# Kernel tuning notes

Hardware: AMD Instinct MI355X
Metric: run time of the kernel (lower is better)

Reference implementation:

```python
import jax, jax.numpy as jnp
import numpy as np

N, E, G, P = 65536, 1048576, 512, 128   # nodes, edges, graphs, nodes per graph
K = 64                                   # sort-pool k (fixed in module)
NUM_CLASSES = 10
FEAT = 128


def _gcn_conv(x, W, b, src, dst):
    # PyG GCNConv: linear, add self-loops, symmetric-normalized aggregation, bias
    h = x @ W
    deg = jnp.ones((N,), x.dtype).at[dst].add(1.0)       # self-loop + in-degree
    dinv = jax.lax.rsqrt(deg)
    coef = (dinv[src] * dinv[dst])[:, None]
    agg = jax.ops.segment_sum(h[src] * coef, dst, num_segments=N)
    agg = agg + h * (dinv * dinv)[:, None]               # self-loop messages
    return agg + b


def setup_inputs() -> dict:
    key = jax.random.key(0)
    ks = jax.random.split(key, 12)
    x = jax.random.normal(ks[0], (N, FEAT), jnp.float32)
    src = jax.random.randint(ks[1], (E,), 0, N, dtype=jnp.int32)
    off = jax.random.randint(ks[2], (E,), 0, P, dtype=jnp.int32)
    dst = (src // P) * P + off                           # keep edges intra-graph
    edge_index = jnp.stack([src, dst])
    # balanced batch vector (implicit): node n belongs to graph n // P
    def lin(k, i, o):
        return jax.random.normal(k, (i, o), jnp.float32) / np.float32(np.sqrt(i))
    return {
        "x": x,
        "W1": lin(ks[3], FEAT, 128), "b1": jnp.zeros((128,), jnp.float32),
        "W2": lin(ks[4], 128, 64),   "b2": jnp.zeros((64,), jnp.float32),
        "W3": lin(ks[5], 64, 32),    "b3": jnp.zeros((32,), jnp.float32),
        "W4": lin(ks[6], 32, 32),    "b4": jnp.zeros((32,), jnp.float32),
        "W5": lin(ks[7], 256, 16).T, "b5": jnp.zeros((16,), jnp.float32),   # Conv1d(1,16,256,256)
        "W6": jax.random.normal(ks[8], (32, 16, 5), jnp.float32) * 0.1,      # Conv1d(16,32,5) OIH
        "b6": jnp.zeros((32,), jnp.float32),
        "Wf1": lin(ks[9], 896, 128), "bf1": jnp.zeros((128,), jnp.float32),
        "Wf2": lin(ks[10], 128, NUM_CLASSES), "bf2": jnp.zeros((NUM_CLASSES,), jnp.float32),
        "edge_index": edge_index,
    }


def reference(x, W1, b1, W2, b2, W3, b3, W4, b4, W5, b5, W6, b6,
              Wf1, bf1, Wf2, bf2, edge_index):
    src, dst = edge_index[0], edge_index[1]
    x1 = jnp.tanh(_gcn_conv(x, W1, b1, src, dst))
    x2 = jnp.tanh(_gcn_conv(x1, W2, b2, src, dst))
    x3 = jnp.tanh(_gcn_conv(x2, W3, b3, src, dst))
    x4 = jnp.tanh(_gcn_conv(x3, W4, b4, src, dst))
    h = jnp.concatenate([x1, x2, x3, x4], axis=-1)       # [N, 256]
    C = h.shape[-1]
    # global_sort_pool: balanced graphs of P nodes -> sort desc by last channel, take top-K
    hg = h.reshape(G, P, C)
    order = jnp.argsort(-hg[:, :, -1], axis=1)[:, :K]    # [G, K]
    pooled = jnp.take_along_axis(hg, order[:, :, None], axis=1)   # [G, K, C]
    # Conv1d(1, 16, 256, stride=256): kernel == stride == C, so per-node matmul
    z = jnp.einsum('gtj,cj->gct', pooled, W5) + b5[None, :, None]  # [G,16,64]
    z = jax.nn.relu(z)
    z = z.reshape(G, 16, -1, 2).max(axis=-1)                       # MaxPool1d(2,2) -> [G,16,32]
    z = jax.lax.conv_general_dilated(z, W6, (1,), 'VALID',
                                     dimension_numbers=('NCH', 'OIH', 'NCH'))
    z = jax.nn.relu(z + b6[None, :, None])                          # [G,32,28]
    z = z.reshape(G, -1)                                            # [G,896]
    out = jax.nn.relu(z @ Wf1 + bf1)
    # dropout is identity at eval time
    return jax.nn.log_softmax(out @ Wf2 + bf2, axis=-1)
```

## Files before the change

### kernel.cpp

```cpp
#include <hip/hip_runtime.h>

#define N_EDGES 1048576
#define N_GRAPH 512
#define REG     2560
#define MAXE    2560
#define PAD     64
#define CHUNK   2048
#define SBLK    (N_EDGES / CHUNK)

typedef __attribute__((ext_vector_type(4))) float floatx4;
typedef __attribute__((ext_vector_type(2))) float floatx2;
typedef __attribute__((ext_vector_type(4))) int intx4;

__global__ void zero_kernel(unsigned* __restrict__ p, int n) {
    int i = blockIdx.x * blockDim.x + threadIdx.x;
    if (i < n) p[i] = 0u;
}

__global__ void scatter_kernel(const int* __restrict__ src, const int* __restrict__ dst,
                               unsigned* __restrict__ cnt, unsigned short* __restrict__ ebuf) {
    __shared__ unsigned short sbuf[CHUNK];
    __shared__ unsigned short sg[CHUNK];
    __shared__ unsigned lhist[512];
    __shared__ unsigned lscan[512];
    __shared__ unsigned gbase[512];
    const int t = threadIdx.x;
    lhist[t] = 0; lhist[t + 256] = 0;
    __syncthreads();
    const intx4* s4 = (const intx4*)(src + blockIdx.x * CHUNK) + t * 2;
    const intx4* d4 = (const intx4*)(dst + blockIdx.x * CHUNK) + t * 2;
    unsigned short gg[8], pk[8], rr[8];
#pragma unroll
    for (int h = 0; h < 2; ++h) {
        intx4 sv = s4[h], dv = d4[h];
        int ss[4] = {sv.x, sv.y, sv.z, sv.w};
        int dd[4] = {dv.x, dv.y, dv.z, dv.w};
#pragma unroll
        for (int j = 0; j < 4; ++j) {
            unsigned g = ((unsigned)dd[j]) >> 7;
            gg[h * 4 + j] = (unsigned short)g;
            pk[h * 4 + j] = (unsigned short)((ss[j] & 127) | ((dd[j] & 127) << 8));
            rr[h * 4 + j] = (unsigned short)atomicAdd(&lhist[g], 1u);
        }
    }
    __syncthreads();
    unsigned a0 = lhist[t], a1 = lhist[t + 256];
    lscan[t] = a0; lscan[t + 256] = a1;
    __syncthreads();
    for (int d = 1; d < 512; d <<= 1) {
        unsigned v0 = (t >= d) ? lscan[t - d] : 0u;
        unsigned v1 = (t + 256 >= d) ? lscan[t + 256 - d] : 0u;
        __syncthreads();
        lscan[t] += v0; lscan[t + 256] += v1;
        __syncthreads();
    }
    lscan[t] -= a0; lscan[t + 256] -= a1;
    gbase[t]       = a0 ? atomicAdd(&cnt[(size_t)t * PAD], a0)         : 0u;
    gbase[t + 256] = a1 ? atomicAdd(&cnt[(size_t)(t + 256) * PAD], a1) : 0u;
    __syncthreads();
#pragma unroll
    for (int j = 0; j < 8; ++j) {
        unsigned pos = lscan[gg[j]] + rr[j];
        sbuf[pos] = pk[j]; sg[pos] = gg[j];
    }
    __syncthreads();
    for (int i = t; i < CHUNK; i += 256) {
        unsigned g = sg[i];
        unsigned pos = gbase[g] + (i - lscan[g]);
        if (pos < REG) ebuf[(size_t)g * REG + pos] = sbuf[i];
    }
}

template<int CIN, int COUT>
__device__ void gcn_matmul(const float* Xin, float* Xio,
                           const float* __restrict__ W, int tid)
{
    constexpr int CL  = COUT / 4;
    constexpr int NPT = 128 / (1024 / CL);
    const int grp = tid / CL, cl = tid % CL;

    float acc[NPT][4];
#pragma unroll
    for (int ni = 0; ni < NPT; ++ni)
#pragma unroll
        for (int j = 0; j < 4; ++j) acc[ni][j] = 0.f;

    for (int k = 0; k < CIN; k += 4) {
        floatx4 xv[NPT];
#pragma unroll
        for (int ni = 0; ni < NPT; ++ni)
            xv[ni] = *(const floatx4*)(Xin + (grp * NPT + ni) * CIN + k);
#pragma unroll
        for (int i = 0; i < 4; ++i) {
            floatx4 wv = *(const floatx4*)(W + (k + i) * COUT + cl * 4);
#pragma unroll
            for (int ni = 0; ni < NPT; ++ni)
#pragma unroll
                for (int j = 0; j < 4; ++j)
                    acc[ni][j] += xv[ni][i] * wv[j];
        }
    }
    __syncthreads();
#pragma unroll
    for (int ni = 0; ni < NPT; ++ni) {
        floatx4 v; v[0] = acc[ni][0]; v[1] = acc[ni][1]; v[2] = acc[ni][2]; v[3] = acc[ni][3];
        *(floatx4*)(Xio + (grp * NPT + ni) * COUT + cl * 4) = v;
    }
    __syncthreads();
}

template<int COUT, int CPT>
__device__ void gcn_agg(float* Xio, const float* __restrict__ Bv,
                        const float* __restrict__ dinv, const int* __restrict__ offs,
                        const float* __restrict__ epack, int tid)
{
    constexpr int TPN = COUT / CPT;
    constexpr int TOT = 128 * TPN;
    constexpr int NV  = CPT / 4;
    float v[NV][4];
    if (tid < TOT) {
        const int n = tid / TPN, cb = (tid % TPN) * CPT;
        float a[NV][4];
#pragma unroll
        for (int q = 0; q < NV; ++q)
#pragma unroll
            for (int j = 0; j < 4; ++j) a[q][j] = 0.f;
        const int o0 = offs[n], o1 = offs[n + 1];
        for (int p = o0; p < o1; ++p) {
            floatx2 e = *(const floatx2*)(epack + 2 * p);
            float cf = e[0];
            int s = (int)__float_as_uint(e[1]);
            const float* hr = Xio + s * COUT + cb;
#pragma unroll
            for (int q = 0; q < NV; ++q) {
                floatx4 h = *(const floatx4*)(hr + q * 4);
#pragma unroll
                for (int j = 0; j < 4; ++j) a[q][j] += h[j] * cf;
            }
        }
        float dn = dinv[n], dnn = dn * dn;
#pragma unroll
        for (int q = 0; q < NV; ++q) {
            floatx4 hs = *(const floatx4*)(Xio + n * COUT + cb + q * 4);
            floatx4 bv = *(const floatx4*)(Bv + cb + q * 4);
#pragma unroll
            for (int j = 0; j < 4; ++j) {
                float t2 = a[q][j] + hs[j] * dnn + bv[j];
                t2 = tanhf(t2);
                v[q][j] = fminf(fmaxf(t2, -1.0f), 1.0f);
            }
        }
    }
    __syncthreads();
    if (tid < TOT) {
        const int n = tid / TPN, cb = (tid % TPN) * CPT;
#pragma unroll
        for (int q = 0; q < NV; ++q) {
            floatx4 o; o[0] = v[q][0]; o[1] = v[q][1]; o[2] = v[q][2]; o[3] = v[q][3];
            *(floatx4*)(Xio + n * COUT + cb + q * 4) = o;
        }
    }
    __syncthreads();
}

__global__ __launch_bounds__(1024, 1) void mega_kernel(
    const float* __restrict__ x,
    const float* __restrict__ W1, const float* __restrict__ b1,
    const float* __restrict__ W2, const float* __restrict__ b2,
    const float* __restrict__ W3, const float* __restrict__ b3,
    const float* __restrict__ W4, const float* __restrict__ b4,
    const float* __restrict__ W5, const float* __restrict__ b5,
    const float* __restrict__ W6, const float* __restrict__ b6,
    const float* __restrict__ Wf1, const float* __restrict__ bf1,
    const float* __restrict__ Wf2, const float* __restrict__ bf2,
    const unsigned* __restrict__ cnt, const unsigned short* __restrict__ ebuf,
    float* __restrict__ out)
{
    __shared__ __align__(16) char pool[162048];
    int*   ldeg = (int*)(pool + 0);
    int*   offs = (int*)(pool + 512);
    float* dinv = (float*)(pool + 1040);
    float* key  = (float*)(pool + 1552);
    unsigned short* ord = (unsigned short*)(pool + 2064);
    float* epack = (float*)(pool + 2304);
    float* W5s   = (float*)(pool + 2304);
    float* X1   = (float*)(pool + 22784);
    float* X2   = (float*)(pool + 88320);
    float* X3   = (float*)(pool + 121088);
    float* X4   = (float*)(pool + 137472);
    float* SCR  = (float*)(pool + 153856);
    float* Zs   = SCR;
    float* ZMP  = SCR + 1024;
    float* Z896 = SCR;
    float* PART = SCR + 1024;
    float* FC1  = SCR + 896;
    float* LG   = SCR;

    const int g   = blockIdx.x;
    const int tid = threadIdx.x;
    int cnt_g = (int)cnt[(size_t)g * PAD];
    if (cnt_g > MAXE) cnt_g = MAXE;
    const unsigned short* eg = ebuf + (size_t)g * REG;

    unsigned short ev[3]; int ne = 0;
    for (int e = tid; e < cnt_g; e += 1024) ev[ne++] = eg[e];

    if (tid < 128) ldeg[tid] = 0;
    __syncthreads();
    for (int i = 0; i < ne; ++i) atomicAdd(&ldeg[(ev[i] >> 8) & 127], 1);
    __syncthreads();
    if (tid < 128) offs[tid + 1] = ldeg[tid];
    if (tid == 0)  offs[0] = 0;
    __syncthreads();
    for (int d = 1; d < 128; d <<= 1) {
        int v = 0;
        if (tid < 128 && tid >= d) v = offs[tid + 1 - d];
        __syncthreads();
        if (tid < 128 && tid >= d) offs[tid + 1] += v;
        __syncthreads();
    }
    if (tid < 128) {
        dinv[tid] = 1.0f / sqrtf((float)(1 + ldeg[tid]));
        ldeg[tid] = offs[tid];
    }
    __syncthreads();
    for (int i = 0; i < ne; ++i) {
        int dn_ = (ev[i] >> 8) & 127, sn = ev[i] & 127;
        int p = atomicAdd(&ldeg[dn_], 1);
        floatx2 e; e[0] = dinv[sn] * dinv[dn_]; e[1] = __uint_as_float((unsigned)sn);
        *(floatx2*)(epack + 2 * p) = e;
    }
    const float* xg = x + (size_t)g * 16384;
    for (int idx = tid; idx < 4096; idx += 1024)
        *(floatx4*)(X1 + idx * 4) = *(const floatx4*)(xg + idx * 4);
    __syncthreads();

    gcn_matmul<128, 128>(X1, X1, W1, tid);
    gcn_agg<128, 16>(X1, b1, dinv, offs, epack, tid);
    gcn_matmul<128,  64>(X1, X2, W2, tid);
    gcn_agg< 64,  8>(X2, b2, dinv, offs, epack, tid);
    gcn_matmul< 64,  32>(X2, X3, W3, tid);
    gcn_agg< 32,  8>(X3, b3, dinv, offs, epack, tid);
    gcn_matmul< 32,  32>(X3, X4, W4, tid);
    gcn_agg< 32,  8>(X4, b4, dinv, offs, epack, tid);

    if (tid < 128) key[tid] = X4[tid * 32 + 31];
    if (tid < 64)  ord[tid] = (unsigned short)tid;
    __syncthreads();
    for (int idx = tid; idx < 4096; idx += 1024) W5s[idx] = W5[idx];
    __syncthreads();
    if (tid < 128) {
        float myk = key[tid];
        int r = 0;
        for (int j = 0; j < 128; ++j) {
            float kj = key[j];
            r += (kj > myk) || (kj == myk && j < tid);
        }
        if (r < 64) ord[r] = (unsigned short)tid;
    }
    __syncthreads();

    {
        int q = tid >> 6, t = tid & 63;
        int node = ord[t] & 127;
        float z0 = b5[q];
        const float* w5a = W5s + q * 256;
        floatx4 zv = {0.f, 0.f, 0.f, 0.f};
        for (int jj = 0; jj < 32; ++jj) {
            int j = (jj + t) & 31;
            floatx4 pv = *(const floatx4*)(X1 + node * 128 + j * 4);
            floatx4 wv = *(const floatx4*)(w5a + j * 4);
#pragma unroll
            for (int u = 0; u < 4; ++u) zv[u] += pv[u] * wv[u];
        }
        for (int jj = 0; jj < 16; ++jj) {
            int j = (jj + t) & 15;
            floatx4 pv = *(const floatx4*)(X2 + node * 64 + j * 4);
            floatx4 wv = *(const floatx4*)(w5a + 128 + j * 4);
#pragma unroll
            for (int u = 0; u < 4; ++u) zv[u] += pv[u] * wv[u];
        }
        for (int jj = 0; jj < 8; ++jj) {
            int j = (jj + t) & 7;
            floatx4 pv = *(const floatx4*)(X3 + node * 32 + j * 4);
            floatx4 wv = *(const floatx4*)(w5a + 192 + j * 4);
#pragma unroll
            for (int u = 0; u < 4; ++u) zv[u] += pv[u] * wv[u];
        }
        for (int jj = 0; jj < 8; ++jj) {
            int j = (jj + t) & 7;
            floatx4 pv = *(const floatx4*)(X4 + node * 32 + j * 4);
            floatx4 wv = *(const floatx4*)(w5a + 224 + j * 4);
#pragma unroll
            for (int u = 0; u < 4; ++u) zv[u] += pv[u] * wv[u];
        }
        z0 += zv[0] + zv[1] + zv[2] + zv[3];
        Zs[q * 64 + t] = fmaxf(z0, 0.f);
    }
    __syncthreads();
    if (tid < 512) {
        int c = tid >> 5, p = tid & 31;
        ZMP[c * 32 + p] = fmaxf(Zs[c * 64 + 2 * p], Zs[c * 64 + 2 * p + 1]);
    }
    __syncthreads();
    for (int idx = tid; idx < 2560; idx += 1024) W5s[idx] = W6[idx];
    __syncthreads();
    if (tid < 896) {
        int oc = tid / 28, p = tid % 28;
        float s = b6[oc];
#pragma unroll
        for (int i = 0; i < 16; ++i) {
            const float* wrow = W5s + (oc * 16 + i) * 5;
#pragma unroll
            for (int k = 0; k < 5; ++k)
                s += ZMP[i * 32 + p + k] * wrow[k];
        }
        Z896[tid] = fmaxf(s, 0.f);
    }
    __syncthreads();
    {
        int f = tid & 127, q = tid >> 7;
        float s = 0.f;
        for (int i = q * 112; i < (q + 1) * 112; ++i)
            s += Z896[i] * Wf1[i * 128 + f];
        PART[q * 128 + f] = s;
    }
    __syncthreads();
    if (tid < 128) {
        float s = bf1[tid];
#pragma unroll
        for (int q = 0; q < 8; ++q) s += PART[q * 128 + tid];
        FC1[tid] = fmaxf(s, 0.f);
    }
    __syncthreads();
    if (tid < 10) {
        float s = bf2[tid];
        for (int i = 0; i < 128; ++i) s += FC1[i] * Wf2[i * 10 + tid];
        LG[tid] = s;
    }
    __syncthreads();
    if (tid == 0) {
        float mx = LG[0];
        for (int i = 1; i < 10; ++i) mx = fmaxf(mx, LG[i]);
        float se = 0.f;
        for (int i = 0; i < 10; ++i) se += expf(LG[i] - mx);
        LG[16] = mx + logf(se);
    }
    __syncthreads();
    if (tid < 10)
        out[g * 10 + tid] = LG[tid] - LG[16];
}

extern "C" void kernel_launch(void* const* d_in, const int* in_sizes, int n_in,
                              void* d_out, int out_size, void* d_ws, size_t ws_size,
                              hipStream_t stream) {
    (void)in_sizes; (void)n_in; (void)out_size; (void)ws_size;
    const float* x   = (const float*)d_in[0];
    const float* W1  = (const float*)d_in[1];
    const float* b1  = (const float*)d_in[2];
    const float* W2  = (const float*)d_in[3];
    const float* b2  = (const float*)d_in[4];
    const float* W3  = (const float*)d_in[5];
    const float* b3  = (const float*)d_in[6];
    const float* W4  = (const float*)d_in[7];
    const float* b4  = (const float*)d_in[8];
    const float* W5  = (const float*)d_in[9];
    const float* b5  = (const float*)d_in[10];
    const float* W6  = (const float*)d_in[11];
    const float* b6  = (const float*)d_in[12];
    const float* Wf1 = (const float*)d_in[13];
    const float* bf1 = (const float*)d_in[14];
    const float* Wf2 = (const float*)d_in[15];
    const float* bf2 = (const float*)d_in[16];
    const int* ei  = (const int*)d_in[17];
    const int* src = ei;
    const int* dst = ei + N_EDGES;

    char* ws = (char*)d_ws;
    unsigned* cnt         = (unsigned*)(ws);
    unsigned short* ebuf  = (unsigned short*)(ws + 131072);

    zero_kernel<<<32, 1024, 0, stream>>>(cnt, 512 * PAD);
    scatter_kernel<<<SBLK, 256, 0, stream>>>(src, dst, cnt, ebuf);
    mega_kernel<<<N_GRAPH, 1024, 0, stream>>>(x, W1, b1, W2, b2, W3, b3, W4, b4,
                                              W5, b5, W6, b6, Wf1, bf1, Wf2, bf2,
                                              cnt, ebuf, (float*)d_out);
}
```

Baseline: 298.4 us.

## Replace global atomic edge bucketing with per-chunk run table and fuse GCN matmul+aggregate

```diff
diff --git a/kernel.cpp b/kernel.cpp
--- a/kernel.cpp
+++ b/kernel.cpp
@@ -2,9 +2,7 @@
 
 #define N_EDGES 1048576
 #define N_GRAPH 512
-#define REG     2560
 #define MAXE    2560
-#define PAD     64
 #define CHUNK   2048
 #define SBLK    (N_EDGES / CHUNK)
 
@@ -12,23 +10,18 @@
 typedef __attribute__((ext_vector_type(2))) float floatx2;
 typedef __attribute__((ext_vector_type(4))) int intx4;
 
-__global__ void zero_kernel(unsigned* __restrict__ p, int n) {
-    int i = blockIdx.x * blockDim.x + threadIdx.x;
-    if (i < n) p[i] = 0u;
-}
-
 __global__ void scatter_kernel(const int* __restrict__ src, const int* __restrict__ dst,
-                               unsigned* __restrict__ cnt, unsigned short* __restrict__ ebuf) {
+                               unsigned* __restrict__ cstab, unsigned short* __restrict__ ebuf) {
     __shared__ unsigned short sbuf[CHUNK];
     __shared__ unsigned short sg[CHUNK];
     __shared__ unsigned lhist[512];
     __shared__ unsigned lscan[512];
-    __shared__ unsigned gbase[512];
     const int t = threadIdx.x;
+    const int b = blockIdx.x;
     lhist[t] = 0; lhist[t + 256] = 0;
     __syncthreads();
-    const intx4* s4 = (const intx4*)(src + blockIdx.x * CHUNK) + t * 2;
-    const intx4* d4 = (const intx4*)(dst + blockIdx.x * CHUNK) + t * 2;
+    const intx4* s4 = (const intx4*)(src + b * CHUNK) + t * 2;
+    const intx4* d4 = (const intx4*)(dst + b * CHUNK) + t * 2;
     unsigned short gg[8], pk[8], rr[8];
 #pragma unroll
     for (int h = 0; h < 2; ++h) {
@@ -55,8 +48,8 @@
         __syncthreads();
     }
     lscan[t] -= a0; lscan[t + 256] -= a1;
-    gbase[t]       = a0 ? atomicAdd(&cnt[(size_t)t * PAD], a0)         : 0u;
-    gbase[t + 256] = a1 ? atomicAdd(&cnt[(size_t)(t + 256) * PAD], a1) : 0u;
+    cstab[(size_t)t * SBLK + b]         = (a0 << 16) | lscan[t];
+    cstab[(size_t)(t + 256) * SBLK + b] = (a1 << 16) | lscan[t + 256];
     __syncthreads();
 #pragma unroll
     for (int j = 0; j < 8; ++j) {
@@ -64,16 +57,16 @@
         sbuf[pos] = pk[j]; sg[pos] = gg[j];
     }
     __syncthreads();
-    for (int i = t; i < CHUNK; i += 256) {
-        unsigned g = sg[i];
-        unsigned pos = gbase[g] + (i - lscan[g]);
-        if (pos < REG) ebuf[(size_t)g * REG + pos] = sbuf[i];
-    }
+    for (int i = t; i < CHUNK; i += 256)
+        ebuf[(size_t)b * CHUNK + i] = sbuf[i];
+    (void)sg;
 }
 
 template<int CIN, int COUT>
-__device__ void gcn_matmul(const float* Xin, float* Xio,
-                           const float* __restrict__ W, int tid)
+__device__ void gcn_layer(const float* Xin, float* Xio,
+                          const float* __restrict__ W, const float* __restrict__ Bv,
+                          const float* __restrict__ dinv, const int* __restrict__ offs,
+                          const float* __restrict__ epack, int tid)
 {
     constexpr int CL  = COUT / 4;
     constexpr int NPT = 128 / (1024 / CL);
@@ -107,58 +100,32 @@
         *(floatx4*)(Xio + (grp * NPT + ni) * COUT + cl * 4) = v;
     }
     __syncthreads();
-}
-
-template<int COUT, int CPT>
-__device__ void gcn_agg(float* Xio, const float* __restrict__ Bv,
-                        const float* __restrict__ dinv, const int* __restrict__ offs,
-                        const float* __restrict__ epack, int tid)
-{
-    constexpr int TPN = COUT / CPT;
-    constexpr int TOT = 128 * TPN;
-    constexpr int NV  = CPT / 4;
-    float v[NV][4];
-    if (tid < TOT) {
-        const int n = tid / TPN, cb = (tid % TPN) * CPT;
-        float a[NV][4];
-#pragma unroll
-        for (int q = 0; q < NV; ++q)
-#pragma unroll
-            for (int j = 0; j < 4; ++j) a[q][j] = 0.f;
-        const int o0 = offs[n], o1 = offs[n + 1];
+
+    floatx4 bv = *(const floatx4*)(Bv + cl * 4);
+    float vout[NPT][4];
+#pragma unroll
+    for (int ni = 0; ni < NPT; ++ni) {
+        int n = grp * NPT + ni;
+        float a[4] = {0.f, 0.f, 0.f, 0.f};
+        int o0 = offs[n], o1 = offs[n + 1];
         for (int p = o0; p < o1; ++p) {
             floatx2 e = *(const floatx2*)(epack + 2 * p);
             float cf = e[0];
             int s = (int)__float_as_uint(e[1]);
-            const float* hr = Xio + s * COUT + cb;
-#pragma unroll
-            for (int q = 0; q < NV; ++q) {
-                floatx4 h = *(const floatx4*)(hr + q * 4);
-#pragma unroll
-                for (int j = 0; j < 4; ++j) a[q][j] += h[j] * cf;
-            }
+            floatx4 h = *(const floatx4*)(Xio + s * COUT + cl * 4);
+#pragma unroll
+            for (int j = 0; j < 4; ++j) a[j] += h[j] * cf;
         }
         float dn = dinv[n], dnn = dn * dn;
 #pragma unroll
-        for (int q = 0; q < NV; ++q) {
-            floatx4 hs = *(const floatx4*)(Xio + n * COUT + cb + q * 4);
-            floatx4 bv = *(const floatx4*)(Bv + cb + q * 4);
-#pragma unroll
-            for (int j = 0; j < 4; ++j) {
-                float t2 = a[q][j] + hs[j] * dnn + bv[j];
-                t2 = tanhf(t2);
-                v[q][j] = fminf(fmaxf(t2, -1.0f), 1.0f);
-            }
-        }
-    }
-    __syncthreads();
-    if (tid < TOT) {
-        const int n = tid / TPN, cb = (tid % TPN) * CPT;
-#pragma unroll
-        for (int q = 0; q < NV; ++q) {
-            floatx4 o; o[0] = v[q][0]; o[1] = v[q][1]; o[2] = v[q][2]; o[3] = v[q][3];
-            *(floatx4*)(Xio + n * COUT + cb + q * 4) = o;
-        }
+        for (int j = 0; j < 4; ++j)
+            vout[ni][j] = tanhf(a[j] + acc[ni][j] * dnn + bv[j]);
+    }
+    __syncthreads();
+#pragma unroll
+    for (int ni = 0; ni < NPT; ++ni) {
+        floatx4 v; v[0] = vout[ni][0]; v[1] = vout[ni][1]; v[2] = vout[ni][2]; v[3] = vout[ni][3];
+        *(floatx4*)(Xio + (grp * NPT + ni) * COUT + cl * 4) = v;
     }
     __syncthreads();
 }
@@ -173,7 +140,7 @@
     const float* __restrict__ W6, const float* __restrict__ b6,
     const float* __restrict__ Wf1, const float* __restrict__ bf1,
     const float* __restrict__ Wf2, const float* __restrict__ bf2,
-    const unsigned* __restrict__ cnt, const unsigned short* __restrict__ ebuf,
+    const unsigned* __restrict__ cstab, const unsigned short* __restrict__ ebuf,
     float* __restrict__ out)
 {
     __shared__ __align__(16) char pool[162048];
@@ -198,51 +165,64 @@
 
     const int g   = blockIdx.x;
     const int tid = threadIdx.x;
-    int cnt_g = (int)cnt[(size_t)g * PAD];
-    if (cnt_g > MAXE) cnt_g = MAXE;
-    const unsigned short* eg = ebuf + (size_t)g * REG;
-
-    unsigned short ev[3]; int ne = 0;
-    for (int e = tid; e < cnt_g; e += 1024) ev[ne++] = eg[e];
+
+    int myc = 0;
+    unsigned short ev[24];
+    if (tid < SBLK) {
+        unsigned cs = cstab[(size_t)g * SBLK + tid];
+        int start = (int)(cs & 0xFFFFu);
+        myc = (int)(cs >> 16);
+        if (myc > 24) myc = 24;
+        const unsigned short* run = ebuf + (size_t)tid * CHUNK + start;
+#pragma unroll
+        for (int w = 0; w < 24; ++w)
+            ev[w] = (w < myc) ? run[w] : (unsigned short)0;
+    }
 
     if (tid < 128) ldeg[tid] = 0;
     __syncthreads();
-    for (int i = 0; i < ne; ++i) atomicAdd(&ldeg[(ev[i] >> 8) & 127], 1);
-    __syncthreads();
-    if (tid < 128) offs[tid + 1] = ldeg[tid];
-    if (tid == 0)  offs[0] = 0;
-    __syncthreads();
-    for (int d = 1; d < 128; d <<= 1) {
-        int v = 0;
-        if (tid < 128 && tid >= d) v = offs[tid + 1 - d];
-        __syncthreads();
-        if (tid < 128 && tid >= d) offs[tid + 1] += v;
-        __syncthreads();
-    }
-    if (tid < 128) {
-        dinv[tid] = 1.0f / sqrtf((float)(1 + ldeg[tid]));
-        ldeg[tid] = offs[tid];
-    }
-    __syncthreads();
-    for (int i = 0; i < ne; ++i) {
-        int dn_ = (ev[i] >> 8) & 127, sn = ev[i] & 127;
-        int p = atomicAdd(&ldeg[dn_], 1);
-        floatx2 e; e[0] = dinv[sn] * dinv[dn_]; e[1] = __uint_as_float((unsigned)sn);
-        *(floatx2*)(epack + 2 * p) = e;
-    }
+#pragma unroll
+    for (int w = 0; w < 24; ++w)
+        if (w < myc) atomicAdd(&ldeg[(ev[w] >> 8) & 127], 1);
+    __syncthreads();
+    if (tid < 64) {
+        int v0 = ldeg[2 * tid], v1 = ldeg[2 * tid + 1];
+        int s = v0 + v1;
+        for (int d = 1; d < 64; d <<= 1) {
+            int u = __shfl_up(s, d, 64);
+            if (tid >= d) s += u;
+        }
+        int e1 = s - v1, e2 = s;
+        offs[2 * tid + 1] = (e1 < MAXE) ? e1 : MAXE;
+        offs[2 * tid + 2] = (e2 < MAXE) ? e2 : MAXE;
+        if (tid == 0) offs[0] = 0;
+    }
+    if (tid >= 128 && tid < 256) {
+        int n = tid - 128;
+        dinv[n] = 1.0f / sqrtf((float)(1 + ldeg[n]));
+    }
+    __syncthreads();
+    if (tid < 128) ldeg[tid] = offs[tid];
+    __syncthreads();
+#pragma unroll
+    for (int w = 0; w < 24; ++w)
+        if (w < myc) {
+            int dn_ = (ev[w] >> 8) & 127, sn = ev[w] & 127;
+            int p = atomicAdd(&ldeg[dn_], 1);
+            if (p < MAXE) {
+                floatx2 e; e[0] = dinv[sn] * dinv[dn_]; e[1] = __uint_as_float((unsigned)sn);
+                *(floatx2*)(epack + 2 * p) = e;
+            }
+        }
     const float* xg = x + (size_t)g * 16384;
     for (int idx = tid; idx < 4096; idx += 1024)
         *(floatx4*)(X1 + idx * 4) = *(const floatx4*)(xg + idx * 4);
     __syncthreads();
 
-    gcn_matmul<128, 128>(X1, X1, W1, tid);
-    gcn_agg<128, 16>(X1, b1, dinv, offs, epack, tid);
-    gcn_matmul<128,  64>(X1, X2, W2, tid);
-    gcn_agg< 64,  8>(X2, b2, dinv, offs, epack, tid);
-    gcn_matmul< 64,  32>(X2, X3, W3, tid);
-    gcn_agg< 32,  8>(X3, b3, dinv, offs, epack, tid);
-    gcn_matmul< 32,  32>(X3, X4, W4, tid);
-    gcn_agg< 32,  8>(X4, b4, dinv, offs, epack, tid);
+    gcn_layer<128, 128>(X1, X1, W1, b1, dinv, offs, epack, tid);
+    gcn_layer<128,  64>(X1, X2, W2, b2, dinv, offs, epack, tid);
+    gcn_layer< 64,  32>(X2, X3, W3, b3, dinv, offs, epack, tid);
+    gcn_layer< 32,  32>(X3, X4, W4, b4, dinv, offs, epack, tid);
 
     if (tid < 128) key[tid] = X4[tid * 32 + 31];
     if (tid < 64)  ord[tid] = (unsigned short)tid;
@@ -377,12 +357,11 @@
     const int* dst = ei + N_EDGES;
 
     char* ws = (char*)d_ws;
-    unsigned* cnt         = (unsigned*)(ws);
-    unsigned short* ebuf  = (unsigned short*)(ws + 131072);
-
-    zero_kernel<<<32, 1024, 0, stream>>>(cnt, 512 * PAD);
-    scatter_kernel<<<SBLK, 256, 0, stream>>>(src, dst, cnt, ebuf);
+    unsigned short* ebuf = (unsigned short*)(ws);
+    unsigned*       cstab = (unsigned*)(ws + 2097152);
+
+    scatter_kernel<<<SBLK, 256, 0, stream>>>(src, dst, cstab, ebuf);
     mega_kernel<<<N_GRAPH, 1024, 0, stream>>>(x, W1, b1, W2, b2, W3, b3, W4, b4,
                                               W5, b5, W6, b6, Wf1, bf1, Wf2, bf2,
-                                              cnt, ebuf, (float*)d_out);
+                                              cstab, ebuf, (float*)d_out);
 }
```

New measurement: 279.1 us. -6.5%, faster.
